# Optimization experiments

Hardware: AMD Instinct MI355X
Metric: run time of the kernel (lower is better)

Reference implementation:

```python
import jax, jax.numpy as jnp
import numpy as np

K = 20          # motif length
A = 21          # alphabet size (amino acids + stop)
U = 600         # number of profiles
NTILES, N, F, TILE = 16, 8, 6, 334
EPS = 1e-6


def setup_inputs() -> dict:
    key = jax.random.key(0)
    kx, kp, kq = jax.random.split(key, 3)
    # X: one-hot encoded translated sequence tiles (ntiles, N, f, tile_size, alphabet)
    ids = jax.random.randint(kx, (NTILES, N, F, TILE), 0, A)
    X = jax.nn.one_hot(ids, A, dtype=jnp.float32)
    # P: softmaxed profile probabilities (k, alphabet, U) -- call() expects softmaxed P
    P = jax.nn.softmax(jax.random.normal(kp, (K, A, U), dtype=jnp.float32) * 2.0, axis=1)
    # Q: background amino-acid distribution (alphabet,)
    Q = jax.nn.softmax(jax.random.normal(kq, (A,), dtype=jnp.float32))
    return {"X": X, "P": P, "Q": Q}


def reference(X, P, Q):
    # R = log(max(P / Q, eps))  -> log-odds filter, shape (k, A, U)
    R = jnp.log(jnp.maximum(P / Q[None, :, None], EPS))
    t, n, f, L0, a = X.shape
    # tf.nn.conv2d with filter (k, A, 1, U) over (tile_size, A) windows ==
    # 1D cross-correlation over length with alphabet as input channels.
    Xf = X.reshape(t * n * f, L0, a)                      # (B, W, C_in=A)
    Z = jax.lax.conv_general_dilated(
        Xf, R, window_strides=(1,), padding='VALID',
        dimension_numbers=('NWC', 'WIO', 'NWC'))          # (B, L0-k+1, U)
    Z = Z.reshape(t, n, f, L0 - K + 1, U)                 # (ntiles, N, f, L, U)
    S = jnp.max(Z, axis=(2, 3))                           # (ntiles, N, U)
    return S, R, Z
```

## Files before the change

### kernel.cpp

```cpp
#include <hip/hip_runtime.h>
#include <stdint.h>

#define NB 768
#define LTILE 334
#define LOUT 315
#define KF 20
#define AA 21
#define UU 600
#define S_SIZE 76800
#define R_SIZE 252000
#define NROWS 420

#define WS_IDS_OFF 504064
#define WS_PS_OFF  (504064 + 258112)

typedef float v2f __attribute__((ext_vector_type(2)));

__global__ __launch_bounds__(256) void prep_R(const float* __restrict__ P,
                                              const float* __restrict__ Q,
                                              float* __restrict__ Rout,
                                              uint16_t* __restrict__ Rb) {
  int i = blockIdx.x * 256 + threadIdx.x;
  if (i >= R_SIZE) return;
  int a = (i / UU) % AA;
  float v = logf(fmaxf(P[i] / Q[a], 1e-6f));
  Rout[i] = v;
  uint32_t x = __float_as_uint(v);
  uint32_t r = (x + 0x7fffu + ((x >> 16) & 1u)) >> 16;
  Rb[i] = (uint16_t)r;
}

__global__ __launch_bounds__(256) void prep_ids(const float* __restrict__ X,
                                                uint8_t* __restrict__ ids) {
  int b = blockIdx.x;
  for (int pos = threadIdx.x; pos < 336; pos += 256) {
    uint8_t id = 0;
    if (pos < LTILE) {
      const float* xp = X + ((size_t)b * LTILE + pos) * AA;
#pragma unroll
      for (int a = 0; a < AA; a++)
        if (xp[a] > 0.5f) id = (uint8_t)a;
    }
    ids[b * 336 + pos] = id;
  }
}

__global__ __launch_bounds__(256, 3) void zmain(const uint16_t* __restrict__ Rb,
                                                const uint8_t* __restrict__ ids,
                                                float* __restrict__ Z,
                                                float* __restrict__ pS) {
  __shared__ __align__(16) uint16_t Tl[NROWS * 64];
  int b = blockIdx.x;
  int u0 = blockIdx.y * 64;
  int uw = min(64, UU - u0);
  int nseg = uw >> 3;
  int tid = threadIdx.x;

  for (int i = tid; i < NROWS * nseg; i += 256) {
    int row = i / nseg, seg = i - row * nseg;
    *(uint4*)(&Tl[row * 64 + seg * 8]) =
        *(const uint4*)(Rb + row * UU + u0 + seg * 8);
  }
  __syncthreads();

  int wave = tid >> 6;
  int lane = tid & 63;
  int seg = lane & 7;
  int lrow = lane >> 3;
  bool segok = seg < nseg;
  const uint8_t* idb = ids + b * 336;
  const char* Tseg = (const char*)Tl + seg * 16;

  v2f sm[4];
#pragma unroll
  for (int d = 0; d < 4; d++) sm[d] = (v2f){-3.4e38f, -3.4e38f};

  for (int pass = 0; pass < 10; pass++) {
    int l = pass * 32 + wave * 8 + lrow;
    if (l < LOUT && segok) {
      int al = l & ~3;
      int sh = (l & 3) * 8;
      const uint32_t* wp = (const uint32_t*)(idb + al);
      uint32_t raw[6];
#pragma unroll
      for (int j = 0; j < 6; j++) raw[j] = wp[j];
      uint32_t W[5];
#pragma unroll
      for (int j = 0; j < 5; j++)
        W[j] = (uint32_t)((((uint64_t)raw[j + 1] << 32) | raw[j]) >> sh);

      v2f acc[4];
#pragma unroll
      for (int d = 0; d < 4; d++) acc[d] = (v2f){0.0f, 0.0f};

#pragma unroll
      for (int w = 0; w < KF; w++) {
        uint32_t c = (W[w >> 2] >> ((w & 3) * 8)) & 0xFFu;
        const uint4 rv = *(const uint4*)(Tseg + (c << 7) + w * 2688);
        acc[0] += (v2f){__uint_as_float(rv.x << 16),
                        __uint_as_float(rv.x & 0xffff0000u)};
        acc[1] += (v2f){__uint_as_float(rv.y << 16),
                        __uint_as_float(rv.y & 0xffff0000u)};
        acc[2] += (v2f){__uint_as_float(rv.z << 16),
                        __uint_as_float(rv.z & 0xffff0000u)};
        acc[3] += (v2f){__uint_as_float(rv.w << 16),
                        __uint_as_float(rv.w & 0xffff0000u)};
      }

      float* zp = Z + ((size_t)b * LOUT + l) * UU + u0 + seg * 8;
      *(float4*)zp = make_float4(acc[0][0], acc[0][1], acc[1][0], acc[1][1]);
      *(float4*)(zp + 4) =
          make_float4(acc[2][0], acc[2][1], acc[3][0], acc[3][1]);
#pragma unroll
      for (int d = 0; d < 4; d++) {
        sm[d][0] = fmaxf(sm[d][0], acc[d][0]);
        sm[d][1] = fmaxf(sm[d][1], acc[d][1]);
      }
    }
  }

#pragma unroll
  for (int d = 0; d < 4; d++) {
#pragma unroll
    for (int off = 8; off <= 32; off <<= 1) {
      sm[d][0] = fmaxf(sm[d][0], __shfl_xor(sm[d][0], off));
      sm[d][1] = fmaxf(sm[d][1], __shfl_xor(sm[d][1], off));
    }
  }

  __syncthreads();
  float* red = (float*)Tl;
  if (lane < 8) {
    float* rp = red + wave * 64 + lane * 8;
    *(float4*)rp = make_float4(sm[0][0], sm[0][1], sm[1][0], sm[1][1]);
    *(float4*)(rp + 4) = make_float4(sm[2][0], sm[2][1], sm[3][0], sm[3][1]);
  }
  __syncthreads();
  if (tid < 64 && tid < uw) {
    float v = red[tid];
#pragma unroll
    for (int w2 = 1; w2 < 4; w2++) v = fmaxf(v, red[w2 * 64 + tid]);
    pS[(size_t)b * UU + u0 + tid] = v;
  }
}

__global__ __launch_bounds__(256) void finalS(const float* __restrict__ pS,
                                              float* __restrict__ S) {
  int i = blockIdx.x * 256 + threadIdx.x;
  if (i >= S_SIZE) return;
  int u = i % UU;
  int tn = i / UU;
  float m = -3.4e38f;
#pragma unroll
  for (int f = 0; f < 6; f++) m = fmaxf(m, pS[(tn * 6 + f) * UU + u]);
  S[i] = m;
}

extern "C" void kernel_launch(void* const* d_in, const int* in_sizes, int n_in,
                              void* d_out, int out_size, void* d_ws, size_t ws_size,
                              hipStream_t stream) {
  const float* X = (const float*)d_in[0];
  const float* P = (const float*)d_in[1];
  const float* Q = (const float*)d_in[2];
  float* S = (float*)d_out;
  float* R = S + S_SIZE;
  float* Z = R + R_SIZE;
  uint16_t* Rb = (uint16_t*)d_ws;
  uint8_t* ids = (uint8_t*)d_ws + WS_IDS_OFF;
  float* pS = (float*)((uint8_t*)d_ws + WS_PS_OFF);

  hipLaunchKernelGGL(prep_R, dim3((R_SIZE + 255) / 256), dim3(256), 0, stream,
                     P, Q, R, Rb);
  hipLaunchKernelGGL(prep_ids, dim3(NB), dim3(256), 0, stream, X, ids);
  hipLaunchKernelGGL(zmain, dim3(NB, 10), dim3(256), 0, stream, Rb, ids, Z, pS);
  hipLaunchKernelGGL(finalS, dim3((S_SIZE + 255) / 256), dim3(256), 0, stream,
                     pS, S);
}
```

Before: 804.8 us.

## Loop over profile groups in one block with register-prefetched LDS tiles

The zmain grid shrinks from (768,10) to 768 blocks, and each block now loops over all ten 64-wide profile groups. While one group is being computed, the next group's bf16 filter slice is held in registers (14 uint4 per thread) and is written to LDS after a barrier, which hides the global load latency. The per-block shared-memory max reduction is replaced by per-wave partial maxima written to global memory, and finalS now folds 24 values per output instead of 6. The risks are higher register pressure under launch bounds of 3, fewer blocks available to hide latency, and a larger partial-max buffer in the workspace.

```diff
diff --git a/kernel.cpp b/kernel.cpp
--- a/kernel.cpp
+++ b/kernel.cpp
@@ -45,106 +45,139 @@
   }
 }
 
+template <int NSEG>
+__device__ __forceinline__ void issue_loads(const uint16_t* __restrict__ Rb,
+                                            int u0, int tid, uint4 (&pref)[14]) {
+#pragma unroll
+  for (int k = 0; k < 14; k++) {
+    int i = tid + k * 256;
+    if (i < NROWS * NSEG) {
+      int row, s;
+      if (NSEG == 8) {
+        row = i >> 3; s = i & 7;
+      } else {
+        row = (i * 0x5556) >> 16;
+        s = i - row * 3;
+      }
+      pref[k] = *(const uint4*)(Rb + row * UU + u0 + s * 8);
+    }
+  }
+}
+
+template <int NSEG>
+__device__ __forceinline__ void write_lds(uint16_t* Tl, int tid,
+                                          const uint4 (&pref)[14]) {
+#pragma unroll
+  for (int k = 0; k < 14; k++) {
+    int i = tid + k * 256;
+    if (i < NROWS * NSEG) {
+      int row, s;
+      if (NSEG == 8) {
+        row = i >> 3; s = i & 7;
+      } else {
+        row = (i * 0x5556) >> 16;
+        s = i - row * 3;
+      }
+      *(uint4*)((char*)Tl + row * 128 + s * 16) = pref[k];
+    }
+  }
+}
+
 __global__ __launch_bounds__(256, 3) void zmain(const uint16_t* __restrict__ Rb,
                                                 const uint8_t* __restrict__ ids,
                                                 float* __restrict__ Z,
-                                                float* __restrict__ pS) {
+                                                float* __restrict__ pS2) {
   __shared__ __align__(16) uint16_t Tl[NROWS * 64];
   int b = blockIdx.x;
-  int u0 = blockIdx.y * 64;
-  int uw = min(64, UU - u0);
-  int nseg = uw >> 3;
   int tid = threadIdx.x;
-
-  for (int i = tid; i < NROWS * nseg; i += 256) {
-    int row = i / nseg, seg = i - row * nseg;
-    *(uint4*)(&Tl[row * 64 + seg * 8]) =
-        *(const uint4*)(Rb + row * UU + u0 + seg * 8);
-  }
-  __syncthreads();
-
   int wave = tid >> 6;
   int lane = tid & 63;
   int seg = lane & 7;
   int lrow = lane >> 3;
-  bool segok = seg < nseg;
   const uint8_t* idb = ids + b * 336;
   const char* Tseg = (const char*)Tl + seg * 16;
 
-  v2f sm[4];
-#pragma unroll
-  for (int d = 0; d < 4; d++) sm[d] = (v2f){-3.4e38f, -3.4e38f};
-
-  for (int pass = 0; pass < 10; pass++) {
-    int l = pass * 32 + wave * 8 + lrow;
-    if (l < LOUT && segok) {
-      int al = l & ~3;
-      int sh = (l & 3) * 8;
-      const uint32_t* wp = (const uint32_t*)(idb + al);
-      uint32_t raw[6];
-#pragma unroll
-      for (int j = 0; j < 6; j++) raw[j] = wp[j];
-      uint32_t W[5];
-#pragma unroll
-      for (int j = 0; j < 5; j++)
-        W[j] = (uint32_t)((((uint64_t)raw[j + 1] << 32) | raw[j]) >> sh);
-
-      v2f acc[4];
-#pragma unroll
-      for (int d = 0; d < 4; d++) acc[d] = (v2f){0.0f, 0.0f};
-
-#pragma unroll
-      for (int w = 0; w < KF; w++) {
-        uint32_t c = (W[w >> 2] >> ((w & 3) * 8)) & 0xFFu;
-        const uint4 rv = *(const uint4*)(Tseg + (c << 7) + w * 2688);
-        acc[0] += (v2f){__uint_as_float(rv.x << 16),
-                        __uint_as_float(rv.x & 0xffff0000u)};
-        acc[1] += (v2f){__uint_as_float(rv.y << 16),
-                        __uint_as_float(rv.y & 0xffff0000u)};
-        acc[2] += (v2f){__uint_as_float(rv.z << 16),
-                        __uint_as_float(rv.z & 0xffff0000u)};
-        acc[3] += (v2f){__uint_as_float(rv.w << 16),
-                        __uint_as_float(rv.w & 0xffff0000u)};
-      }
-
-      float* zp = Z + ((size_t)b * LOUT + l) * UU + u0 + seg * 8;
-      *(float4*)zp = make_float4(acc[0][0], acc[0][1], acc[1][0], acc[1][1]);
-      *(float4*)(zp + 4) =
-          make_float4(acc[2][0], acc[2][1], acc[3][0], acc[3][1]);
-#pragma unroll
-      for (int d = 0; d < 4; d++) {
-        sm[d][0] = fmaxf(sm[d][0], acc[d][0]);
-        sm[d][1] = fmaxf(sm[d][1], acc[d][1]);
-      }
-    }
-  }
-
-#pragma unroll
-  for (int d = 0; d < 4; d++) {
-#pragma unroll
-    for (int off = 8; off <= 32; off <<= 1) {
-      sm[d][0] = fmaxf(sm[d][0], __shfl_xor(sm[d][0], off));
-      sm[d][1] = fmaxf(sm[d][1], __shfl_xor(sm[d][1], off));
-    }
-  }
-
-  __syncthreads();
-  float* red = (float*)Tl;
-  if (lane < 8) {
-    float* rp = red + wave * 64 + lane * 8;
-    *(float4*)rp = make_float4(sm[0][0], sm[0][1], sm[1][0], sm[1][1]);
-    *(float4*)(rp + 4) = make_float4(sm[2][0], sm[2][1], sm[3][0], sm[3][1]);
-  }
-  __syncthreads();
-  if (tid < 64 && tid < uw) {
-    float v = red[tid];
-#pragma unroll
-    for (int w2 = 1; w2 < 4; w2++) v = fmaxf(v, red[w2 * 64 + tid]);
-    pS[(size_t)b * UU + u0 + tid] = v;
-  }
-}
-
-__global__ __launch_bounds__(256) void finalS(const float* __restrict__ pS,
+  uint4 pref[14];
+  issue_loads<8>(Rb, 0, tid, pref);
+
+  for (int ug = 0; ug < 10; ug++) {
+    int nseg = (ug < 9) ? 8 : 3;
+    int u0 = ug * 64;
+
+    __syncthreads();
+    if (nseg == 8) write_lds<8>(Tl, tid, pref);
+    else           write_lds<3>(Tl, tid, pref);
+    if (ug + 1 < 9)       issue_loads<8>(Rb, u0 + 64, tid, pref);
+    else if (ug + 1 == 9) issue_loads<3>(Rb, u0 + 64, tid, pref);
+    __syncthreads();
+
+    bool segok = seg < nseg;
+
+    v2f sm[4];
+#pragma unroll
+    for (int d = 0; d < 4; d++) sm[d] = (v2f){-3.4e38f, -3.4e38f};
+
+    for (int pass = 0; pass < 10; pass++) {
+      int l = pass * 32 + wave * 8 + lrow;
+      if (l < LOUT && segok) {
+        int al = l & ~3;
+        int sh = (l & 3) * 8;
+        const uint32_t* wp = (const uint32_t*)(idb + al);
+        uint32_t raw[6];
+#pragma unroll
+        for (int j = 0; j < 6; j++) raw[j] = wp[j];
+        uint32_t W[5];
+#pragma unroll
+        for (int j = 0; j < 5; j++)
+          W[j] = (uint32_t)((((uint64_t)raw[j + 1] << 32) | raw[j]) >> sh);
+
+        v2f acc[4];
+#pragma unroll
+        for (int d = 0; d < 4; d++) acc[d] = (v2f){0.0f, 0.0f};
+
+#pragma unroll
+        for (int w = 0; w < KF; w++) {
+          uint32_t c = (W[w >> 2] >> ((w & 3) * 8)) & 0xFFu;
+          const uint4 rv = *(const uint4*)(Tseg + (c << 7) + w * 2688);
+          acc[0] += (v2f){__uint_as_float(rv.x << 16),
+                          __uint_as_float(rv.x & 0xffff0000u)};
+          acc[1] += (v2f){__uint_as_float(rv.y << 16),
+                          __uint_as_float(rv.y & 0xffff0000u)};
+          acc[2] += (v2f){__uint_as_float(rv.z << 16),
+                          __uint_as_float(rv.z & 0xffff0000u)};
+          acc[3] += (v2f){__uint_as_float(rv.w << 16),
+                          __uint_as_float(rv.w & 0xffff0000u)};
+        }
+
+        float* zp = Z + ((size_t)b * LOUT + l) * UU + u0 + seg * 8;
+        *(float4*)zp = make_float4(acc[0][0], acc[0][1], acc[1][0], acc[1][1]);
+        *(float4*)(zp + 4) =
+            make_float4(acc[2][0], acc[2][1], acc[3][0], acc[3][1]);
+#pragma unroll
+        for (int d = 0; d < 4; d++) {
+          sm[d][0] = fmaxf(sm[d][0], acc[d][0]);
+          sm[d][1] = fmaxf(sm[d][1], acc[d][1]);
+        }
+      }
+    }
+
+#pragma unroll
+    for (int d = 0; d < 4; d++) {
+#pragma unroll
+      for (int off = 8; off <= 32; off <<= 1) {
+        sm[d][0] = fmaxf(sm[d][0], __shfl_xor(sm[d][0], off));
+        sm[d][1] = fmaxf(sm[d][1], __shfl_xor(sm[d][1], off));
+      }
+    }
+    if (lrow == 0 && seg < nseg) {
+      float* rp = pS2 + ((size_t)(b * 4 + wave)) * UU + u0 + seg * 8;
+      *(float4*)rp = make_float4(sm[0][0], sm[0][1], sm[1][0], sm[1][1]);
+      *(float4*)(rp + 4) = make_float4(sm[2][0], sm[2][1], sm[3][0], sm[3][1]);
+    }
+  }
+}
+
+__global__ __launch_bounds__(256) void finalS(const float* __restrict__ pS2,
                                               float* __restrict__ S) {
   int i = blockIdx.x * 256 + threadIdx.x;
   if (i >= S_SIZE) return;
@@ -152,7 +185,10 @@
   int tn = i / UU;
   float m = -3.4e38f;
 #pragma unroll
-  for (int f = 0; f < 6; f++) m = fmaxf(m, pS[(tn * 6 + f) * UU + u]);
+  for (int f = 0; f < 6; f++)
+#pragma unroll
+    for (int w = 0; w < 4; w++)
+      m = fmaxf(m, pS2[((size_t)((tn * 6 + f) * 4 + w)) * UU + u]);
   S[i] = m;
 }
 
@@ -167,12 +203,12 @@
   float* Z = R + R_SIZE;
   uint16_t* Rb = (uint16_t*)d_ws;
   uint8_t* ids = (uint8_t*)d_ws + WS_IDS_OFF;
-  float* pS = (float*)((uint8_t*)d_ws + WS_PS_OFF);
+  float* pS2 = (float*)((uint8_t*)d_ws + WS_PS_OFF);
 
   hipLaunchKernelGGL(prep_R, dim3((R_SIZE + 255) / 256), dim3(256), 0, stream,
                      P, Q, R, Rb);
   hipLaunchKernelGGL(prep_ids, dim3(NB), dim3(256), 0, stream, X, ids);
-  hipLaunchKernelGGL(zmain, dim3(NB, 10), dim3(256), 0, stream, Rb, ids, Z, pS);
+  hipLaunchKernelGGL(zmain, dim3(NB), dim3(256), 0, stream, Rb, ids, Z, pS2);
   hipLaunchKernelGGL(finalS, dim3((S_SIZE + 255) / 256), dim3(256), 0, stream,
-                     pS, S);
-}
+                     pS2, S);
+}
```

Result: slower. 892.8 us (+10.9%).
